# Optimization experiments

Measured on AMD Instinct MI355X. Metric: run time of the kernel, lower is better.

The kernel has to match this reference:

```python
import jax, jax.numpy as jnp
import numpy as np

N, C_IN, C_OUT = 8192, 256, 128
TEMP = 1.0
EDGE_P = 0.01  # Bernoulli edge probability -> avg degree ~82


def setup_inputs() -> dict:
    key = jax.random.key(0)
    k_x, k_adj, k_w, k_v0, k_v1 = jax.random.split(key, 5)
    node_feats = jax.random.normal(k_x, (N, C_IN), dtype=jnp.float32)
    adj_matrix = (jax.random.uniform(k_adj, (N, N)) < EDGE_P).astype(jnp.float32)
    lim_w = np.sqrt(6.0 / (C_IN + C_OUT))
    W = jax.random.uniform(k_w, (C_IN, C_OUT), minval=-lim_w, maxval=lim_w, dtype=jnp.float32)
    b = jnp.zeros((C_OUT,), dtype=jnp.float32)
    lim_v = np.sqrt(6.0 / (C_OUT + 1))
    v0 = jax.random.uniform(k_v0, (C_OUT,), minval=-lim_v, maxval=lim_v, dtype=jnp.float32)
    v1 = jax.random.uniform(k_v1, (C_OUT,), minval=-lim_v, maxval=lim_v, dtype=jnp.float32)
    return {"node_feats": node_feats, "adj_matrix": adj_matrix, "W": W, "b": b, "v0": v0, "v1": v1}


def reference(node_feats, adj_matrix, W, b, v0, v1):
    # h: [N, c_out]
    h = node_feats @ W + b
    f1 = h @ v0  # [N]
    f2 = h @ v1  # [N]
    # attn_logits = adj * (f1_i + f2_j); adj==0 entries become exact zeros,
    # which torch's .to_sparse() drops -> sparse softmax normalizes only
    # over edges (adj != 0), and empty rows densify to all-zero rows.
    logits = adj_matrix * (f1[:, None] + f2[None, :])
    vals = (jax.nn.sigmoid(logits) - 0.5) / TEMP
    mask = adj_matrix != 0
    masked = jnp.where(mask, vals, -jnp.inf)
    row_max = jnp.max(masked, axis=1, keepdims=True)
    row_max = jnp.where(jnp.isfinite(row_max), row_max, 0.0)  # guard empty rows
    e = jnp.where(mask, jnp.exp(masked - row_max), 0.0)
    denom = jnp.sum(e, axis=1, keepdims=True)
    attn_probs = e / jnp.maximum(denom, jnp.finfo(e.dtype).tiny)  # empty rows -> 0
    return attn_probs @ h
```

## Files before the change

kernel.cpp:

```cpp
#include <hip/hip_runtime.h>
#include <math.h>

#define NN    8192
#define CIN   256
#define COUT  128
#define MAXEG 256

typedef unsigned uvec4 __attribute__((ext_vector_type(4)));

__global__ __launch_bounds__(256) void k1_gemm(
    const float* __restrict__ X, const float* __restrict__ W,
    const float* __restrict__ b, const float* __restrict__ v0,
    const float* __restrict__ v1,
    float* __restrict__ h, float* __restrict__ f1, float* __restrict__ f2)
{
    __shared__ float Xs[16][32];
    const int tid = threadIdx.x;
    const int ct  = tid & 63;
    const int rg  = tid >> 6;
    const int c   = ct * 2;
    const int row0 = blockIdx.x * 16;

    float acc[4][2] = {{0.f,0.f},{0.f,0.f},{0.f,0.f},{0.f,0.f}};

    for (int kc = 0; kc < CIN; kc += 32) {
        if (tid < 128) {
            const int r = tid >> 3, q = tid & 7;
            const float4 xv = *(const float4*)(X + (size_t)(row0 + r) * CIN + kc + q * 4);
            *(float4*)&Xs[r][q * 4] = xv;
        }
        float2 wv[32];
        #pragma unroll
        for (int kk = 0; kk < 32; ++kk)
            wv[kk] = *(const float2*)(W + (size_t)(kc + kk) * COUT + c);
        __syncthreads();

        #pragma unroll
        for (int rr = 0; rr < 4; ++rr) {
            const int lr = rg * 4 + rr;
            #pragma unroll
            for (int k4 = 0; k4 < 8; ++k4) {
                const float4 xv = *(const float4*)&Xs[lr][k4 * 4];
                acc[rr][0] += xv.x * wv[k4*4+0].x; acc[rr][1] += xv.x * wv[k4*4+0].y;
                acc[rr][0] += xv.y * wv[k4*4+1].x; acc[rr][1] += xv.y * wv[k4*4+1].y;
                acc[rr][0] += xv.z * wv[k4*4+2].x; acc[rr][1] += xv.z * wv[k4*4+2].y;
                acc[rr][0] += xv.w * wv[k4*4+3].x; acc[rr][1] += xv.w * wv[k4*4+3].y;
            }
        }
        __syncthreads();
    }

    const float b0 = b[c], b1 = b[c+1];
    const float v00 = v0[c], v01 = v0[c+1];
    const float v10 = v1[c], v11 = v1[c+1];

    #pragma unroll
    for (int rr = 0; rr < 4; ++rr) {
        const int row = row0 + rg * 4 + rr;
        const float h0 = acc[rr][0] + b0;
        const float h1 = acc[rr][1] + b1;
        *(float2*)(h + (size_t)row * COUT + c) = make_float2(h0, h1);
        float p0 = h0 * v00 + h1 * v01;
        float p1 = h0 * v10 + h1 * v11;
        #pragma unroll
        for (int off = 32; off; off >>= 1) {
            p0 += __shfl_down(p0, off, 64);
            p1 += __shfl_down(p1, off, 64);
        }
        if (ct == 0) { f1[row] = p0; f2[row] = p1; }
    }
}

__global__ __launch_bounds__(256) void k_scan(
    const float* __restrict__ adj, unsigned* __restrict__ cnt,
    unsigned* __restrict__ outw)
{
    __shared__ unsigned short sjl[4][MAXEG];
    const int tid  = threadIdx.x;
    const int wid  = tid >> 6;
    const int lane = tid & 63;
    const int row  = blockIdx.x * 4 + wid;
    const uvec4* rowp = (const uvec4*)(adj + (size_t)row * NN);
    unsigned wcnt = 0;

    #pragma unroll
    for (int b = 0; b < 4; ++b) {
        uvec4 v[8];
        #pragma unroll
        for (int it = 0; it < 8; ++it)
            v[it] = __builtin_nontemporal_load(rowp + b * 512 + it * 64 + lane);

        unsigned lm = 0;
        #pragma unroll
        for (int it = 0; it < 8; ++it) {
            const unsigned m4 = ((v[it].x >> 23) & 1u) | ((v[it].y >> 22) & 2u) |
                                ((v[it].z >> 21) & 4u) | ((v[it].w >> 20) & 8u);
            lm |= m4 << (it * 4);
        }

        const int lc = __popc(lm);
        int pre = lc;
        #pragma unroll
        for (int off = 1; off < 64; off <<= 1) {
            const int t = __shfl_up(pre, off, 64);
            if (lane >= off) pre += t;
        }
        unsigned basep = wcnt + (unsigned)(pre - lc);
        wcnt += (unsigned)__shfl(pre, 63, 64);

        unsigned mm = lm;
        while (mm) {
            const int bit = __builtin_ctz(mm);
            mm &= mm - 1;
            const unsigned j = (unsigned)((b * 512 + (bit >> 2) * 64 + lane) * 4 + (bit & 3));
            if (basep < MAXEG) sjl[wid][basep] = (unsigned short)j;
            ++basep;
        }
    }

    asm volatile("s_waitcnt lgkmcnt(0)" ::: "memory");
    #pragma unroll
    for (int r = 0; r < 2; ++r) {
        const int k = lane + r * 64;
        const unsigned w = (unsigned)sjl[wid][2 * k] | ((unsigned)sjl[wid][2 * k + 1] << 16);
        outw[(size_t)row * 128 + k] = w;
    }
    if (lane == 0) cnt[row] = min(wcnt, (unsigned)MAXEG);
}

__global__ __launch_bounds__(256) void kB(
    const float* __restrict__ h, const float* __restrict__ f1,
    const float* __restrict__ f2, const unsigned* __restrict__ cnt,
    float* __restrict__ out)
{
    __shared__ unsigned short jl[4][MAXEG];
    __shared__ float vl[4][MAXEG];
    const int tid  = threadIdx.x;
    const int wid  = tid >> 6;
    const int lane = tid & 63;
    const int i    = blockIdx.x * 4 + wid;
    const int n    = (int)cnt[i];
    const int c    = lane * 2;

    if (n == 0) {
        *(float2*)(out + (size_t)i * COUT + c) = make_float2(0.f, 0.f);
        return;
    }

    #pragma unroll
    for (int r = 0; r < 2; ++r) {
        const int k = lane + r * 64;
        const unsigned w = ((const unsigned*)out)[(size_t)i * 128 + k];
        jl[wid][2 * k]     = (unsigned short)(w & 0xffffu);
        jl[wid][2 * k + 1] = (unsigned short)(w >> 16);
    }
    asm volatile("s_waitcnt lgkmcnt(0)" ::: "memory");

    const float f1i = f1[i];
    float m = -1e30f;
    #pragma unroll
    for (int q = 0; q < 4; ++q) {
        const int p = lane + q * 64;
        if (p < n) {
            const float x = f1i + f2[jl[wid][p]];
            const float s = 1.f / (1.f + __expf(-x)) - 0.5f;
            vl[wid][p] = s;
            m = fmaxf(m, s);
        }
    }
    #pragma unroll
    for (int off = 32; off; off >>= 1) m = fmaxf(m, __shfl_xor(m, off, 64));

    float ssum = 0.f;
    #pragma unroll
    for (int q = 0; q < 4; ++q) {
        const int p = lane + q * 64;
        if (p < n) {
            const float e = __expf(vl[wid][p] - m);
            vl[wid][p] = e;
            ssum += e;
        }
    }
    #pragma unroll
    for (int off = 32; off; off >>= 1) ssum += __shfl_xor(ssum, off, 64);
    const float inv = 1.f / ssum;
    asm volatile("s_waitcnt lgkmcnt(0)" ::: "memory");

    float ax = 0.f, ay = 0.f;
    int p = 0;
    for (; p + 3 < n; p += 4) {
        const int   j0 = jl[wid][p],     j1 = jl[wid][p + 1];
        const int   j2 = jl[wid][p + 2], j3 = jl[wid][p + 3];
        const float w0 = vl[wid][p],     w1 = vl[wid][p + 1];
        const float w2 = vl[wid][p + 2], w3 = vl[wid][p + 3];
        const float2 a0 = *(const float2*)(h + (size_t)j0 * COUT + c);
        const float2 a1 = *(const float2*)(h + (size_t)j1 * COUT + c);
        const float2 a2 = *(const float2*)(h + (size_t)j2 * COUT + c);
        const float2 a3 = *(const float2*)(h + (size_t)j3 * COUT + c);
        ax += w0 * a0.x + w1 * a1.x + w2 * a2.x + w3 * a3.x;
        ay += w0 * a0.y + w1 * a1.y + w2 * a2.y + w3 * a3.y;
    }
    for (; p < n; ++p) {
        const int   j = jl[wid][p];
        const float w = vl[wid][p];
        const float2 a = *(const float2*)(h + (size_t)j * COUT + c);
        ax += w * a.x;
        ay += w * a.y;
    }
    *(float2*)(out + (size_t)i * COUT + c) = make_float2(ax * inv, ay * inv);
}

extern "C" void kernel_launch(void* const* d_in, const int* in_sizes, int n_in,
                              void* d_out, int out_size, void* d_ws, size_t ws_size,
                              hipStream_t stream) {
    const float* X   = (const float*)d_in[0];
    const float* adj = (const float*)d_in[1];
    const float* W   = (const float*)d_in[2];
    const float* b   = (const float*)d_in[3];
    const float* v0  = (const float*)d_in[4];
    const float* v1  = (const float*)d_in[5];
    float* out = (float*)d_out;

    float*    h   = (float*)d_ws;
    float*    f1  = h + (size_t)NN * COUT;
    float*    f2  = f1 + NN;
    unsigned* cnt = (unsigned*)(f2 + NN);

    k1_gemm<<<NN / 16, 256, 0, stream>>>(X, W, b, v0, v1, h, f1, f2);
    k_scan<<<NN / 4, 256, 0, stream>>>(adj, cnt, (unsigned*)out);
    kB<<<NN / 4, 256, 0, stream>>>(h, f1, f2, cnt, out);
}
```

Measured before the change: 99.79 us.

## Fuse adjacency scan with softmax-aggregate kernel and double-buffer row loads

Merges the adjacency compaction kernel and the softmax/aggregation kernel into one, so neighbour indices stay in shared memory. This removes the round trip through the output buffer, the count array and one kernel launch. Adjacency row loads are now double-buffered in registers, with plain loads replacing nontemporal ones, to overlap loading with mask processing. The gather loop is unrolled to 8 for more memory parallelism. The costs are higher register pressure and less occupancy, and the gather phase can no longer overlap with other blocks' streaming in a separate launch.

```diff
diff --git a/kernel.cpp b/kernel.cpp
--- a/kernel.cpp
+++ b/kernel.cpp
@@ -71,25 +71,24 @@
     }
 }
 
-__global__ __launch_bounds__(256) void k_scan(
-    const float* __restrict__ adj, unsigned* __restrict__ cnt,
-    unsigned* __restrict__ outw)
+__global__ __launch_bounds__(256) void k2_fused(
+    const float* __restrict__ adj, const float* __restrict__ h,
+    const float* __restrict__ f1, const float* __restrict__ f2,
+    float* __restrict__ out)
 {
     __shared__ unsigned short sjl[4][MAXEG];
+    __shared__ float vl[4][MAXEG];
+
     const int tid  = threadIdx.x;
     const int wid  = tid >> 6;
     const int lane = tid & 63;
     const int row  = blockIdx.x * 4 + wid;
-    const uvec4* rowp = (const uvec4*)(adj + (size_t)row * NN);
+    const uvec4* rowp = (const uvec4*)(adj + (size_t)row * NN) + lane;
+
     unsigned wcnt = 0;
-
-    #pragma unroll
-    for (int b = 0; b < 4; ++b) {
-        uvec4 v[8];
-        #pragma unroll
-        for (int it = 0; it < 8; ++it)
-            v[it] = __builtin_nontemporal_load(rowp + b * 512 + it * 64 + lane);
-
+    uvec4 va[8], vb[8];
+
+    auto process = [&](const uvec4 (&v)[8], const int b) {
         unsigned lm = 0;
         #pragma unroll
         for (int it = 0; it < 8; ++it) {
@@ -97,7 +96,6 @@
                                 ((v[it].z >> 21) & 4u) | ((v[it].w >> 20) & 8u);
             lm |= m4 << (it * 4);
         }
-
         const int lc = __popc(lm);
         int pre = lc;
         #pragma unroll
@@ -107,7 +105,6 @@
         }
         unsigned basep = wcnt + (unsigned)(pre - lc);
         wcnt += (unsigned)__shfl(pre, 63, 64);
-
         unsigned mm = lm;
         while (mm) {
             const int bit = __builtin_ctz(mm);
@@ -116,53 +113,37 @@
             if (basep < MAXEG) sjl[wid][basep] = (unsigned short)j;
             ++basep;
         }
+    };
+
+    #pragma unroll
+    for (int it = 0; it < 8; ++it) va[it] = rowp[0 * 512 + it * 64];
+    #pragma unroll
+    for (int it = 0; it < 8; ++it) vb[it] = rowp[1 * 512 + it * 64];
+    process(va, 0);
+    #pragma unroll
+    for (int it = 0; it < 8; ++it) va[it] = rowp[2 * 512 + it * 64];
+    process(vb, 1);
+    #pragma unroll
+    for (int it = 0; it < 8; ++it) vb[it] = rowp[3 * 512 + it * 64];
+    process(va, 2);
+    process(vb, 3);
+
+    const int n = min((int)wcnt, MAXEG);
+    const int c = lane * 2;
+    if (n == 0) {
+        *(float2*)(out + (size_t)row * COUT + c) = make_float2(0.f, 0.f);
+        return;
     }
 
     asm volatile("s_waitcnt lgkmcnt(0)" ::: "memory");
-    #pragma unroll
-    for (int r = 0; r < 2; ++r) {
-        const int k = lane + r * 64;
-        const unsigned w = (unsigned)sjl[wid][2 * k] | ((unsigned)sjl[wid][2 * k + 1] << 16);
-        outw[(size_t)row * 128 + k] = w;
-    }
-    if (lane == 0) cnt[row] = min(wcnt, (unsigned)MAXEG);
-}
-
-__global__ __launch_bounds__(256) void kB(
-    const float* __restrict__ h, const float* __restrict__ f1,
-    const float* __restrict__ f2, const unsigned* __restrict__ cnt,
-    float* __restrict__ out)
-{
-    __shared__ unsigned short jl[4][MAXEG];
-    __shared__ float vl[4][MAXEG];
-    const int tid  = threadIdx.x;
-    const int wid  = tid >> 6;
-    const int lane = tid & 63;
-    const int i    = blockIdx.x * 4 + wid;
-    const int n    = (int)cnt[i];
-    const int c    = lane * 2;
-
-    if (n == 0) {
-        *(float2*)(out + (size_t)i * COUT + c) = make_float2(0.f, 0.f);
-        return;
-    }
-
-    #pragma unroll
-    for (int r = 0; r < 2; ++r) {
-        const int k = lane + r * 64;
-        const unsigned w = ((const unsigned*)out)[(size_t)i * 128 + k];
-        jl[wid][2 * k]     = (unsigned short)(w & 0xffffu);
-        jl[wid][2 * k + 1] = (unsigned short)(w >> 16);
-    }
-    asm volatile("s_waitcnt lgkmcnt(0)" ::: "memory");
-
-    const float f1i = f1[i];
+
+    const float f1i = f1[row];
     float m = -1e30f;
     #pragma unroll
     for (int q = 0; q < 4; ++q) {
         const int p = lane + q * 64;
         if (p < n) {
-            const float x = f1i + f2[jl[wid][p]];
+            const float x = f1i + f2[sjl[wid][p]];
             const float s = 1.f / (1.f + __expf(-x)) - 0.5f;
             vl[wid][p] = s;
             m = fmaxf(m, s);
@@ -188,26 +169,25 @@
 
     float ax = 0.f, ay = 0.f;
     int p = 0;
-    for (; p + 3 < n; p += 4) {
-        const int   j0 = jl[wid][p],     j1 = jl[wid][p + 1];
-        const int   j2 = jl[wid][p + 2], j3 = jl[wid][p + 3];
-        const float w0 = vl[wid][p],     w1 = vl[wid][p + 1];
-        const float w2 = vl[wid][p + 2], w3 = vl[wid][p + 3];
-        const float2 a0 = *(const float2*)(h + (size_t)j0 * COUT + c);
-        const float2 a1 = *(const float2*)(h + (size_t)j1 * COUT + c);
-        const float2 a2 = *(const float2*)(h + (size_t)j2 * COUT + c);
-        const float2 a3 = *(const float2*)(h + (size_t)j3 * COUT + c);
-        ax += w0 * a0.x + w1 * a1.x + w2 * a2.x + w3 * a3.x;
-        ay += w0 * a0.y + w1 * a1.y + w2 * a2.y + w3 * a3.y;
+    for (; p + 7 < n; p += 8) {
+        int   jj[8];
+        float ww[8];
+        float2 aa[8];
+        #pragma unroll
+        for (int u = 0; u < 8; ++u) { jj[u] = sjl[wid][p + u]; ww[u] = vl[wid][p + u]; }
+        #pragma unroll
+        for (int u = 0; u < 8; ++u) aa[u] = *(const float2*)(h + (size_t)jj[u] * COUT + c);
+        #pragma unroll
+        for (int u = 0; u < 8; ++u) { ax += ww[u] * aa[u].x; ay += ww[u] * aa[u].y; }
     }
     for (; p < n; ++p) {
-        const int   j = jl[wid][p];
+        const int   j = sjl[wid][p];
         const float w = vl[wid][p];
         const float2 a = *(const float2*)(h + (size_t)j * COUT + c);
         ax += w * a.x;
         ay += w * a.y;
     }
-    *(float2*)(out + (size_t)i * COUT + c) = make_float2(ax * inv, ay * inv);
+    *(float2*)(out + (size_t)row * COUT + c) = make_float2(ax * inv, ay * inv);
 }
 
 extern "C" void kernel_launch(void* const* d_in, const int* in_sizes, int n_in,
@@ -221,12 +201,10 @@
     const float* v1  = (const float*)d_in[5];
     float* out = (float*)d_out;
 
-    float*    h   = (float*)d_ws;
-    float*    f1  = h + (size_t)NN * COUT;
-    float*    f2  = f1 + NN;
-    unsigned* cnt = (unsigned*)(f2 + NN);
+    float* h  = (float*)d_ws;
+    float* f1 = h + (size_t)NN * COUT;
+    float* f2 = f1 + NN;
 
     k1_gemm<<<NN / 16, 256, 0, stream>>>(X, W, b, v0, v1, h, f1, f2);
-    k_scan<<<NN / 4, 256, 0, stream>>>(adj, cnt, (unsigned*)out);
-    kB<<<NN / 4, 256, 0, stream>>>(h, f1, f2, cnt, out);
+    k2_fused<<<NN / 4, 256, 0, stream>>>(adj, h, f1, f2, out);
 }
```

Result: faster. 94.33 us (-5.5%).

## Fuse GEMM and adjacency scan into one launch with block-per-row LDS atomics

Applied to the files above, without the earlier changes.

Merges the feature GEMM and the adjacency compaction into one kernel whose first 512 blocks do the GEMM and the remaining blocks each scan one adjacency row. The scan now uses a whole 256-thread block per row and builds the neighbour list with shared-memory atomics instead of a wave-level prefix scan. This removes one kernel launch and lets the GEMM overlap the bandwidth-bound adjacency read. In exchange, neighbour order within a row is nondeterministic, so floating-point summation order varies between runs.

```diff
diff --git a/kernel.cpp b/kernel.cpp
--- a/kernel.cpp
+++ b/kernel.cpp
@@ -4,128 +4,107 @@
 #define NN    8192
 #define CIN   256
 #define COUT  128
+#define NK1   512
 #define MAXEG 256
 
 typedef unsigned uvec4 __attribute__((ext_vector_type(4)));
 
-__global__ __launch_bounds__(256) void k1_gemm(
-    const float* __restrict__ X, const float* __restrict__ W,
-    const float* __restrict__ b, const float* __restrict__ v0,
-    const float* __restrict__ v1,
-    float* __restrict__ h, float* __restrict__ f1, float* __restrict__ f2)
+__global__ __launch_bounds__(256) void kA(
+    const float* __restrict__ X, const float* __restrict__ adj,
+    const float* __restrict__ W, const float* __restrict__ b,
+    const float* __restrict__ v0, const float* __restrict__ v1,
+    float* __restrict__ h, float* __restrict__ f1, float* __restrict__ f2,
+    unsigned* __restrict__ cnt, unsigned* __restrict__ outw)
 {
     __shared__ float Xs[16][32];
+    __shared__ unsigned scnt;
+    __shared__ unsigned short sjl[MAXEG];
+
     const int tid = threadIdx.x;
-    const int ct  = tid & 63;
-    const int rg  = tid >> 6;
-    const int c   = ct * 2;
-    const int row0 = blockIdx.x * 16;
-
-    float acc[4][2] = {{0.f,0.f},{0.f,0.f},{0.f,0.f},{0.f,0.f}};
-
-    for (int kc = 0; kc < CIN; kc += 32) {
-        if (tid < 128) {
-            const int r = tid >> 3, q = tid & 7;
-            const float4 xv = *(const float4*)(X + (size_t)(row0 + r) * CIN + kc + q * 4);
-            *(float4*)&Xs[r][q * 4] = xv;
-        }
-        float2 wv[32];
-        #pragma unroll
-        for (int kk = 0; kk < 32; ++kk)
-            wv[kk] = *(const float2*)(W + (size_t)(kc + kk) * COUT + c);
-        __syncthreads();
+
+    if (blockIdx.x < NK1) {
+        const int ct  = tid & 63;
+        const int rg  = tid >> 6;
+        const int c   = ct * 2;
+        const int row0 = blockIdx.x * 16;
+
+        float acc[4][2] = {{0.f,0.f},{0.f,0.f},{0.f,0.f},{0.f,0.f}};
+
+        for (int kc = 0; kc < CIN; kc += 32) {
+            if (tid < 128) {
+                const int r = tid >> 3, q = tid & 7;
+                const float4 xv = *(const float4*)(X + (size_t)(row0 + r) * CIN + kc + q * 4);
+                *(float4*)&Xs[r][q * 4] = xv;
+            }
+            float2 wv[32];
+            #pragma unroll
+            for (int kk = 0; kk < 32; ++kk)
+                wv[kk] = *(const float2*)(W + (size_t)(kc + kk) * COUT + c);
+            __syncthreads();
+
+            #pragma unroll
+            for (int rr = 0; rr < 4; ++rr) {
+                const int lr = rg * 4 + rr;
+                #pragma unroll
+                for (int k4 = 0; k4 < 8; ++k4) {
+                    const float4 xv = *(const float4*)&Xs[lr][k4 * 4];
+                    acc[rr][0] += xv.x * wv[k4*4+0].x; acc[rr][1] += xv.x * wv[k4*4+0].y;
+                    acc[rr][0] += xv.y * wv[k4*4+1].x; acc[rr][1] += xv.y * wv[k4*4+1].y;
+                    acc[rr][0] += xv.z * wv[k4*4+2].x; acc[rr][1] += xv.z * wv[k4*4+2].y;
+                    acc[rr][0] += xv.w * wv[k4*4+3].x; acc[rr][1] += xv.w * wv[k4*4+3].y;
+                }
+            }
+            __syncthreads();
+        }
+
+        const float b0 = b[c], b1 = b[c+1];
+        const float v00 = v0[c], v01 = v0[c+1];
+        const float v10 = v1[c], v11 = v1[c+1];
 
         #pragma unroll
         for (int rr = 0; rr < 4; ++rr) {
-            const int lr = rg * 4 + rr;
+            const int row = row0 + rg * 4 + rr;
+            const float h0 = acc[rr][0] + b0;
+            const float h1 = acc[rr][1] + b1;
+            *(float2*)(h + (size_t)row * COUT + c) = make_float2(h0, h1);
+            float p0 = h0 * v00 + h1 * v01;
+            float p1 = h0 * v10 + h1 * v11;
             #pragma unroll
-            for (int k4 = 0; k4 < 8; ++k4) {
-                const float4 xv = *(const float4*)&Xs[lr][k4 * 4];
-                acc[rr][0] += xv.x * wv[k4*4+0].x; acc[rr][1] += xv.x * wv[k4*4+0].y;
-                acc[rr][0] += xv.y * wv[k4*4+1].x; acc[rr][1] += xv.y * wv[k4*4+1].y;
-                acc[rr][0] += xv.z * wv[k4*4+2].x; acc[rr][1] += xv.z * wv[k4*4+2].y;
-                acc[rr][0] += xv.w * wv[k4*4+3].x; acc[rr][1] += xv.w * wv[k4*4+3].y;
-            }
-        }
-        __syncthreads();
-    }
-
-    const float b0 = b[c], b1 = b[c+1];
-    const float v00 = v0[c], v01 = v0[c+1];
-    const float v10 = v1[c], v11 = v1[c+1];
-
-    #pragma unroll
-    for (int rr = 0; rr < 4; ++rr) {
-        const int row = row0 + rg * 4 + rr;
-        const float h0 = acc[rr][0] + b0;
-        const float h1 = acc[rr][1] + b1;
-        *(float2*)(h + (size_t)row * COUT + c) = make_float2(h0, h1);
-        float p0 = h0 * v00 + h1 * v01;
-        float p1 = h0 * v10 + h1 * v11;
-        #pragma unroll
-        for (int off = 32; off; off >>= 1) {
-            p0 += __shfl_down(p0, off, 64);
-            p1 += __shfl_down(p1, off, 64);
-        }
-        if (ct == 0) { f1[row] = p0; f2[row] = p1; }
-    }
-}
-
-__global__ __launch_bounds__(256) void k_scan(
-    const float* __restrict__ adj, unsigned* __restrict__ cnt,
-    unsigned* __restrict__ outw)
-{
-    __shared__ unsigned short sjl[4][MAXEG];
-    const int tid  = threadIdx.x;
-    const int wid  = tid >> 6;
-    const int lane = tid & 63;
-    const int row  = blockIdx.x * 4 + wid;
-    const uvec4* rowp = (const uvec4*)(adj + (size_t)row * NN);
-    unsigned wcnt = 0;
-
-    #pragma unroll
-    for (int b = 0; b < 4; ++b) {
+            for (int off = 32; off; off >>= 1) {
+                p0 += __shfl_down(p0, off, 64);
+                p1 += __shfl_down(p1, off, 64);
+            }
+            if (ct == 0) { f1[row] = p0; f2[row] = p1; }
+        }
+    } else {
+        const int i = blockIdx.x - NK1;
+        const uvec4* rowp = (const uvec4*)(adj + (size_t)i * NN);
         uvec4 v[8];
         #pragma unroll
         for (int it = 0; it < 8; ++it)
-            v[it] = __builtin_nontemporal_load(rowp + b * 512 + it * 64 + lane);
-
-        unsigned lm = 0;
+            v[it] = __builtin_nontemporal_load(rowp + tid + it * 256);
+
+        if (tid == 0) scnt = 0;
+        __syncthreads();
+
         #pragma unroll
         for (int it = 0; it < 8; ++it) {
-            const unsigned m4 = ((v[it].x >> 23) & 1u) | ((v[it].y >> 22) & 2u) |
-                                ((v[it].z >> 21) & 4u) | ((v[it].w >> 20) & 8u);
-            lm |= m4 << (it * 4);
-        }
-
-        const int lc = __popc(lm);
-        int pre = lc;
-        #pragma unroll
-        for (int off = 1; off < 64; off <<= 1) {
-            const int t = __shfl_up(pre, off, 64);
-            if (lane >= off) pre += t;
-        }
-        unsigned basep = wcnt + (unsigned)(pre - lc);
-        wcnt += (unsigned)__shfl(pre, 63, 64);
-
-        unsigned mm = lm;
-        while (mm) {
-            const int bit = __builtin_ctz(mm);
-            mm &= mm - 1;
-            const unsigned j = (unsigned)((b * 512 + (bit >> 2) * 64 + lane) * 4 + (bit & 3));
-            if (basep < MAXEG) sjl[wid][basep] = (unsigned short)j;
-            ++basep;
-        }
-    }
-
-    asm volatile("s_waitcnt lgkmcnt(0)" ::: "memory");
-    #pragma unroll
-    for (int r = 0; r < 2; ++r) {
-        const int k = lane + r * 64;
-        const unsigned w = (unsigned)sjl[wid][2 * k] | ((unsigned)sjl[wid][2 * k + 1] << 16);
-        outw[(size_t)row * 128 + k] = w;
-    }
-    if (lane == 0) cnt[row] = min(wcnt, (unsigned)MAXEG);
+            if (v[it].x | v[it].y | v[it].z | v[it].w) {
+                const int j0 = (tid + it * 256) * 4;
+                if (v[it].x) { const unsigned p = atomicAdd(&scnt, 1u); if (p < MAXEG) sjl[p] = (unsigned short)(j0    ); }
+                if (v[it].y) { const unsigned p = atomicAdd(&scnt, 1u); if (p < MAXEG) sjl[p] = (unsigned short)(j0 + 1); }
+                if (v[it].z) { const unsigned p = atomicAdd(&scnt, 1u); if (p < MAXEG) sjl[p] = (unsigned short)(j0 + 2); }
+                if (v[it].w) { const unsigned p = atomicAdd(&scnt, 1u); if (p < MAXEG) sjl[p] = (unsigned short)(j0 + 3); }
+            }
+        }
+        __syncthreads();
+
+        if (tid < 128) {
+            const unsigned w = (unsigned)sjl[2 * tid] | ((unsigned)sjl[2 * tid + 1] << 16);
+            outw[(size_t)i * 128 + tid] = w;
+        }
+        if (tid == 0) cnt[i] = min(scnt, (unsigned)MAXEG);
+    }
 }
 
 __global__ __launch_bounds__(256) void kB(
@@ -226,7 +205,6 @@
     float*    f2  = f1 + NN;
     unsigned* cnt = (unsigned*)(f2 + NN);
 
-    k1_gemm<<<NN / 16, 256, 0, stream>>>(X, W, b, v0, v1, h, f1, f2);
-    k_scan<<<NN / 4, 256, 0, stream>>>(adj, cnt, (unsigned*)out);
+    kA<<<NK1 + NN, 256, 0, stream>>>(X, adj, W, b, v0, v1, h, f1, f2, cnt, (unsigned*)out);
     kB<<<NN / 4, 256, 0, stream>>>(h, f1, f2, cnt, out);
 }
```

Result: faster. 88.83 us (-11.0%).
